# Kernel tuning notes

Hardware: AMD Instinct MI355X
Metric: run time of the kernel (lower is better)

## Reference

```python
import jax, jax.numpy as jnp
import numpy as np

N_NODES = 40000      # batch of group nodes
DEGREE = 32          # neighbors (members) per node
NUM_USERS = 100000
NUM_GROUPS = 50000
EMBED_DIM = 64


def setup_inputs() -> dict:
    key = jax.random.key(0)
    ks = jax.random.split(key, 8)
    E = N_NODES * DEGREE
    d = EMBED_DIM
    return {
        "nodes": jax.random.randint(ks[0], (N_NODES,), 0, NUM_GROUPS),
        "neigh_idx": jax.random.randint(ks[1], (E,), 0, NUM_USERS),
        # edge i belongs to node segment_ids[i]; sorted, DEGREE edges per node
        "segment_ids": jnp.repeat(jnp.arange(N_NODES), DEGREE),
        "u2e_weight": jax.random.normal(ks[2], (NUM_USERS, d), jnp.float32) * 0.02,
        "g2e_weight": jax.random.normal(ks[3], (NUM_GROUPS, d), jnp.float32) * 0.02,
        "att1_w": jax.random.normal(ks[4], (d, 2 * d), jnp.float32) * (1.0 / np.sqrt(2 * d)),
        "att1_b": jnp.zeros((d,), jnp.float32),
        "att2_w": jax.random.normal(ks[5], (d, d), jnp.float32) * (1.0 / np.sqrt(d)),
        "att2_b": jnp.zeros((d,), jnp.float32),
        "att3_w": jax.random.normal(ks[6], (1, d), jnp.float32) * (1.0 / np.sqrt(d)),
        "att3_b": jnp.zeros((1,), jnp.float32),
    }


def _segment_softmax(logits, seg, num_segments):
    # numerically stable softmax within each node's neighbor segment
    m = jax.ops.segment_max(logits, seg, num_segments=num_segments)
    a = jnp.exp(logits - m[seg])
    s = jax.ops.segment_sum(a, seg, num_segments=num_segments)
    return a / s[seg]


def reference(nodes, neigh_idx, segment_ids, u2e_weight, g2e_weight,
              att1_w, att1_b, att2_w, att2_b, att3_w, att3_b):
    e_u = u2e_weight[neigh_idx]                 # [E, d] member embeddings
    g_rep = g2e_weight[nodes][segment_ids]      # [E, d] group query broadcast per edge
    x = jnp.concatenate([e_u, g_rep], axis=-1)  # [E, 2d]
    h = jax.nn.relu(x @ att1_w.T + att1_b)      # [E, d] (dropout inactive at eval)
    h = jax.nn.relu(h @ att2_w.T + att2_b)      # [E, d]
    logits = (h @ att3_w.T + att3_b)[:, 0]      # [E]
    att = _segment_softmax(logits, segment_ids, N_NODES)  # [E]
    # attention-weighted aggregation of member embeddings per node
    return jax.ops.segment_sum(att[:, None] * e_u, segment_ids, num_segments=N_NODES)  # [N, d]
```

## Files before the change

### kernel.cpp

```cpp
#include <hip/hip_runtime.h>
#include <hip/hip_bf16.h>

typedef __attribute__((ext_vector_type(8))) short short8;
typedef __attribute__((ext_vector_type(4))) float floatx4;
typedef __attribute__((ext_vector_type(2))) float float2v;
typedef __attribute__((ext_vector_type(4))) unsigned int uintx4;

#define NNODES 40000
#define NPW 4
#define WAVES 8
#define NPB (NPW * WAVES)
#define NBLK (NNODES / NPB)

#define U2E_ELEMS (100000 * 64)
#define WS_ALIGN 256
#define WS_NEEDED ((size_t)U2E_ELEMS * 2 + WS_ALIGN)


__device__ __forceinline__ float bf2f(unsigned short s) {
    return __uint_as_float(((unsigned int)s) << 16);
}
__device__ __forceinline__ unsigned short f2bf(float f) {
    unsigned int u = __float_as_uint(f);
    u += 0x7fffu + ((u >> 16) & 1u);
    return (unsigned short)(u >> 16);
}
__device__ __forceinline__ unsigned int pk2bf(float lo, float hi) {
#if __has_builtin(__builtin_amdgcn_cvt_pk_bf16_f32)
    auto r = __builtin_amdgcn_cvt_pk_bf16_f32(lo, hi);
    unsigned int u; __builtin_memcpy(&u, &r, 4);
    return u;
#else
    return (unsigned int)f2bf(lo) | ((unsigned int)f2bf(hi) << 16);
#endif
}
__device__ __forceinline__ short8 cvt8(const float* fp) {
    floatx4 a = *(const floatx4*)fp;
    floatx4 b = *(const floatx4*)(fp + 4);
    uintx4 u;
    u[0] = pk2bf(a[0], a[1]); u[1] = pk2bf(a[2], a[3]);
    u[2] = pk2bf(b[0], b[1]); u[3] = pk2bf(b[2], b[3]);
    short8 r; __builtin_memcpy(&r, &u, 16);
    return r;
}
__device__ __forceinline__ short8 u4s8(uintx4 u) {
    short8 r; __builtin_memcpy(&r, &u, 16);
    return r;
}

__device__ __forceinline__ float2v f2pair(floatx4 v, int i) {
    return (float2v){v[2 * i], v[2 * i + 1]};
}
__device__ __forceinline__ float2v fma2(float2v a, float2v b, float2v c) {
#if __has_builtin(__builtin_elementwise_fma)
    return __builtin_elementwise_fma(a, b, c);
#else
    return (float2v){fmaf(a[0], b[0], c[0]), fmaf(a[1], b[1], c[1])};
#endif
}
__device__ __forceinline__ float2v relu2(float2v a) {
#if __has_builtin(__builtin_elementwise_max)
    return __builtin_elementwise_max(a, (float2v)(0.f));
#else
    return (float2v){fmaxf(a[0], 0.f), fmaxf(a[1], 0.f)};
#endif
}

__global__ __launch_bounds__(256) void convert_u2e(
    const float* __restrict__ u2e, unsigned short* __restrict__ ub) {
    const size_t i = ((size_t)blockIdx.x * 256 + threadIdx.x) * 8;
    if (i < U2E_ELEMS) *(short8*)(ub + i) = cvt8(u2e + i);
}

__device__ __forceinline__ int sigma_row(int dt, int m) {
    return (dt & 1) * 32 + (m >> 2) * 8 + ((dt >> 1) << 2) + (m & 3);
}

template<int PRE>
__global__ __launch_bounds__(512, 4) void gat_fused(
    const int*   __restrict__ nodes,
    const int*   __restrict__ neigh,
    const float* __restrict__ u2f,
    const unsigned short* __restrict__ u2b,
    const float* __restrict__ g2e,
    const float* __restrict__ w1,
    const float* __restrict__ b1,
    const float* __restrict__ w2,
    const float* __restrict__ b2,
    const float* __restrict__ w3,
    float* __restrict__ out)
{
    __shared__ alignas(16) short w1f[16 * 64 * 8];
    __shared__ alignas(16) short w2f[8 * 64 * 8];
    __shared__ alignas(16) short ebuf[WAVES][2048];
    __shared__ alignas(16) float abuf[WAVES][64];
    __shared__ alignas(16) float bvec[192];

    const int tid  = threadIdx.x;
    const int wv   = tid >> 6;
    const int lane = tid & 63;
    const int q    = lane >> 4;
    const int n16  = lane & 15;

    for (int i = tid; i < 16 * 64; i += 512) {
        int s = i >> 6, slot = i & 63;
        int dt = s >> 2, kc = s & 3;
        int row = sigma_row(dt, slot & 15);
        int k   = kc * 32 + (slot >> 4) * 8;
        *(short8*)&w1f[i * 8] = cvt8(w1 + (size_t)row * 128 + k);
    }
    for (int i = tid; i < 8 * 64; i += 512) {
        int s = i >> 6, slot = i & 63;
        int ot = s >> 1, kc = s & 1;
        int row = sigma_row(ot, slot & 15);
        int k   = kc * 32 + (slot >> 4) * 8;
        *(short8*)&w2f[i * 8] = cvt8(w2 + (size_t)row * 64 + k);
    }
    for (int i = tid; i < 192; i += 512)
        bvec[i] = (i < 64) ? b1[i] : (i < 128) ? b2[i - 64] : w3[i - 128];
    __syncthreads();

    const int n0 = blockIdx.x * NPB + wv * NPW;

    const int ew0 = n16 * 64 + ((q ^ (n16 & 7)) * 8);
    const int ew1 = n16 * 64 + (((4 + q) ^ (n16 & 7)) * 8);

    const int hh = lane >> 5;
    const int mm = lane & 31;
    int bofs[8];
    #pragma unroll
    for (int p = 0; p < 8; ++p)
        bofs[p] = hh * 1024 + ((((mm >> 2) ^ p) << 3) + ((mm & 3) << 1));
    const int dimo = (mm << 1) | hh;

    int gn, d0, d1;
    short8 A00, A01, A10, A11, G0, G1;

    auto loadA = [&](int idx, int half) -> short8 {
        if (PRE) return *(const short8*)(u2b + (size_t)idx * 64 + half * 32 + q * 8);
        else     return cvt8(u2f + (size_t)idx * 64 + half * 32 + q * 8);
    };

    {
        int g0i = nodes[n0];
        size_t eb0 = (size_t)n0 * 32;
        int c0 = neigh[eb0 + n16];
        int c1 = neigh[eb0 + 16 + n16];
        A00 = loadA(c0, 0); A01 = loadA(c0, 1);
        A10 = loadA(c1, 0); A11 = loadA(c1, 1);
        G0  = cvt8(g2e + (size_t)g0i * 64 + q * 8);
        G1  = cvt8(g2e + (size_t)g0i * 64 + 32 + q * 8);
        int n1 = n0 + 1;
        gn = nodes[n1];
        size_t eb1 = (size_t)n1 * 32;
        d0 = neigh[eb1 + n16];
        d1 = neigh[eb1 + 16 + n16];
    }

    const floatx4 zero4 = {0.f, 0.f, 0.f, 0.f};
    int qo = q * 8;

    for (int it = 0; it < NPW; ++it) {
        const int n = n0 + it;
        const short8 a00 = A00, a01 = A01, a10 = A10, a11 = A11, g0 = G0, g1 = G1;

        floatx4 acc1[2][4];
        #pragma unroll
        for (int et = 0; et < 2; ++et)
            #pragma unroll
            for (int dt = 0; dt < 4; ++dt) acc1[et][dt] = zero4;
        #pragma unroll
        for (int kc = 0; kc < 4; ++kc) {
            const short8 x0 = (kc == 0) ? a00 : (kc == 1) ? a01 : (kc == 2) ? g0 : g1;
            const short8 x1 = (kc == 0) ? a10 : (kc == 1) ? a11 : (kc == 2) ? g0 : g1;
            #pragma unroll
            for (int dt = 0; dt < 4; ++dt) {
                const short8 w = *(const short8*)&w1f[((dt * 4 + kc) * 64 + lane) * 8];
                acc1[0][dt] = __builtin_amdgcn_mfma_f32_16x16x32_bf16(w, x0, acc1[0][dt], 0, 0, 0);
                acc1[1][dt] = __builtin_amdgcn_mfma_f32_16x16x32_bf16(w, x1, acc1[1][dt], 0, 0, 0);
            }
        }

        {
            short* ebw = &ebuf[wv][0];
            *(short8*)&ebw[ew0]        = a00;
            *(short8*)&ebw[ew1]        = a01;
            *(short8*)&ebw[ew0 + 1024] = a10;
            *(short8*)&ebw[ew1 + 1024] = a11;
        }

        if (it < NPW - 1) {
            A00 = loadA(d0, 0); A01 = loadA(d0, 1);
            A10 = loadA(d1, 0); A11 = loadA(d1, 1);
            G0  = cvt8(g2e + (size_t)gn * 64 + qo);
            G1  = cvt8(g2e + (size_t)gn * 64 + 32 + qo);
            int nn = n0 + it + 2; if (nn > NNODES - 1) nn = NNODES - 1;
            gn = nodes[nn];
            size_t eb2 = (size_t)nn * 32;
            d0 = neigh[eb2 + n16];
            d1 = neigh[eb2 + 16 + n16];
        }

        asm volatile("" : "+v"(qo));

        floatx4 B1[2][2];
        B1[0][0] = *(const floatx4*)&bvec[qo];
        B1[0][1] = *(const floatx4*)&bvec[qo + 4];
        B1[1][0] = *(const floatx4*)&bvec[qo + 32];
        B1[1][1] = *(const floatx4*)&bvec[qo + 36];
        short8 y[2][2];
        #pragma unroll
        for (int kc2 = 0; kc2 < 2; ++kc2)
            #pragma unroll
            for (int et = 0; et < 2; ++et) {
                float2v p0 = relu2(f2pair(acc1[et][kc2], 0)     + f2pair(B1[kc2][0], 0));
                float2v p1 = relu2(f2pair(acc1[et][kc2], 1)     + f2pair(B1[kc2][0], 1));
                float2v p2 = relu2(f2pair(acc1[et][kc2 + 2], 0) + f2pair(B1[kc2][1], 0));
                float2v p3 = relu2(f2pair(acc1[et][kc2 + 2], 1) + f2pair(B1[kc2][1], 1));
                uintx4 u;
                u[0] = pk2bf(p0[0], p0[1]);
                u[1] = pk2bf(p1[0], p1[1]);
                u[2] = pk2bf(p2[0], p2[1]);
                u[3] = pk2bf(p3[0], p3[1]);
                y[kc2][et] = u4s8(u);
            }

        floatx4 acc2[2][4];
        #pragma unroll
        for (int et = 0; et < 2; ++et)
            #pragma unroll
            for (int ot = 0; ot < 4; ++ot) acc2[et][ot] = zero4;
        #pragma unroll
        for (int kc2 = 0; kc2 < 2; ++kc2)
            #pragma unroll
            for (int ot = 0; ot < 4; ++ot) {
                const short8 w = *(const short8*)&w2f[((ot * 2 + kc2) * 64 + lane) * 8];
                acc2[0][ot] = __builtin_amdgcn_mfma_f32_16x16x32_bf16(w, y[kc2][0], acc2[0][ot], 0, 0, 0);
                acc2[1][ot] = __builtin_amdgcn_mfma_f32_16x16x32_bf16(w, y[kc2][1], acc2[1][ot], 0, 0, 0);
            }

        floatx4 B2[2][2], W3[2][2];
        B2[0][0] = *(const floatx4*)&bvec[qo + 64];
        B2[0][1] = *(const floatx4*)&bvec[qo + 68];
        B2[1][0] = *(const floatx4*)&bvec[qo + 96];
        B2[1][1] = *(const floatx4*)&bvec[qo + 100];
        W3[0][0] = *(const floatx4*)&bvec[qo + 128];
        W3[0][1] = *(const floatx4*)&bvec[qo + 132];
        W3[1][0] = *(const floatx4*)&bvec[qo + 160];
        W3[1][1] = *(const floatx4*)&bvec[qo + 164];
        float2v s0v = (float2v)(0.f), s1v = (float2v)(0.f);
        #pragma unroll
        for (int ot = 0; ot < 4; ++ot) {
            const int h = ot & 1, g = ot >> 1;
            const float2v b2a = f2pair(B2[h][g], 0), b2b = f2pair(B2[h][g], 1);
            const float2v w3a = f2pair(W3[h][g], 0), w3b = f2pair(W3[h][g], 1);
            s0v = fma2(relu2(f2pair(acc2[0][ot], 0) + b2a), w3a, s0v);
            s0v = fma2(relu2(f2pair(acc2[0][ot], 1) + b2b), w3b, s0v);
            s1v = fma2(relu2(f2pair(acc2[1][ot], 0) + b2a), w3a, s1v);
            s1v = fma2(relu2(f2pair(acc2[1][ot], 1) + b2b), w3b, s1v);
        }
        float s0 = s0v[0] + s0v[1];
        float s1 = s1v[0] + s1v[1];
        s0 += __shfl_xor(s0, 16, 64); s0 += __shfl_xor(s0, 32, 64);
        s1 += __shfl_xor(s1, 16, 64); s1 += __shfl_xor(s1, 32, 64);
        const float lg = ((lane >> 4) & 1) ? s1 : s0;

        float mx = lg;
        #pragma unroll
        for (int off = 1; off < 32; off <<= 1)
            mx = fmaxf(mx, __shfl_xor(mx, off, 64));
        const float ex = __expf(lg - mx);
        float sm = ex;
        #pragma unroll
        for (int off = 1; off < 32; off <<= 1)
            sm += __shfl_xor(sm, off, 64);
        const float attv = ex / sm;

        *(float2v*)&abuf[wv][mm * 2] = (float2v){attv, attv};
        {
            const short* ebw = &ebuf[wv][0];
            const float* abp = &abuf[wv][hh * 32];
            float2v ac0 = (float2v)(0.f), ac1 = (float2v)(0.f);
            #pragma unroll
            for (int k = 0; k < 16; k += 2) {
                const float2v ap0 = *(const float2v*)&abp[2 * k];
                const float2v ap1 = *(const float2v*)&abp[2 * k + 2];
                const unsigned int u0 = *(const unsigned int*)&ebw[bofs[k & 7] + k * 64];
                const unsigned int u1 = *(const unsigned int*)&ebw[bofs[(k + 1) & 7] + (k + 1) * 64];
                float2v e0, e1;
                e0[0] = __uint_as_float(u0 << 16);
                e0[1] = __uint_as_float(u0 & 0xffff0000u);
                e1[0] = __uint_as_float(u1 << 16);
                e1[1] = __uint_as_float(u1 & 0xffff0000u);
                ac0 = fma2(ap0, e0, ac0);
                ac1 = fma2(ap1, e1, ac1);
            }
            const float2v acp = ac0 + ac1;
            const float lt = acp[0] + __shfl_xor(acp[0], 32, 64);
            const float ht = acp[1] + __shfl_xor(acp[1], 32, 64);
            out[(size_t)n * 64 + dimo] = hh ? ht : lt;
        }
    }
}

extern "C" void kernel_launch(void* const* d_in, const int* in_sizes, int n_in,
                              void* d_out, int out_size, void* d_ws, size_t ws_size,
                              hipStream_t stream) {
    const int*   nodes = (const int*)d_in[0];
    const int*   neigh = (const int*)d_in[1];
    const float* u2e = (const float*)d_in[3];
    const float* g2e = (const float*)d_in[4];
    const float* w1  = (const float*)d_in[5];
    const float* b1  = (const float*)d_in[6];
    const float* w2  = (const float*)d_in[7];
    const float* b2  = (const float*)d_in[8];
    const float* w3  = (const float*)d_in[9];
    float* out = (float*)d_out;

    if (ws_size >= WS_NEEDED) {
        unsigned short* ub = (unsigned short*)(((uintptr_t)d_ws + WS_ALIGN - 1) & ~(uintptr_t)(WS_ALIGN - 1));
        hipLaunchKernelGGL(convert_u2e, dim3((U2E_ELEMS / 8 + 255) / 256), dim3(256),
                           0, stream, u2e, ub);
        hipLaunchKernelGGL(gat_fused<1>, dim3(NBLK), dim3(512), 0, stream,
                           nodes, neigh, u2e, ub, g2e, w1, b1, w2, b2, w3, out);
    } else {
        hipLaunchKernelGGL(gat_fused<0>, dim3(NBLK), dim3(512), 0, stream,
                           nodes, neigh, u2e, (const unsigned short*)nullptr,
                           g2e, w1, b1, w2, b2, w3, out);
    }
}
```

Baseline: 155.9 us.

## Precompute bf16 group table and streamline segment softmax reductions

Adds a pre-pass that converts the group embedding table to bf16 in the workspace, so the fused kernel gathers half-width query rows. The softmax drops the max subtraction and uses DPP and swizzle adds plus a hardware reciprocal instead of shuffle-based max and sum reductions. The LDS reads of member embeddings are moved ahead of the softmax so their latency can overlap. The extra conversion pass reads the whole group table each call, and skipping the max subtraction risks overflow for large logits.

```diff
diff --git a/kernel.cpp b/kernel.cpp
--- a/kernel.cpp
+++ b/kernel.cpp
@@ -13,8 +13,10 @@
 #define NBLK (NNODES / NPB)
 
 #define U2E_ELEMS (100000 * 64)
+#define G2E_ELEMS (50000 * 64)
 #define WS_ALIGN 256
-#define WS_NEEDED ((size_t)U2E_ELEMS * 2 + WS_ALIGN)
+#define WS_NEEDED   ((size_t)U2E_ELEMS * 2 + WS_ALIGN)
+#define WS_NEEDED_G ((size_t)U2E_ELEMS * 2 + (size_t)G2E_ELEMS * 2 + WS_ALIGN)
 
 
 __device__ __forceinline__ float bf2f(unsigned short s) {
@@ -66,23 +68,47 @@
 #endif
 }
 
+template<int CTRL>
+__device__ __forceinline__ float dppadd(float v) {
+#if __has_builtin(__builtin_amdgcn_update_dpp)
+    int y = __builtin_amdgcn_update_dpp(0, __float_as_int(v), CTRL, 0xf, 0xf, true);
+    return v + __int_as_float(y);
+#else
+    return v + __shfl_xor(v, (CTRL == 0xB1) ? 1 : (CTRL == 0x4E) ? 2 : (CTRL == 0x141) ? 4 : 8, 64);
+#endif
+}
+__device__ __forceinline__ float swz16add(float v) {
+#if __has_builtin(__builtin_amdgcn_ds_swizzle)
+    int y = __builtin_amdgcn_ds_swizzle(__float_as_int(v), 0x401F);
+    return v + __int_as_float(y);
+#else
+    return v + __shfl_xor(v, 16, 64);
+#endif
+}
+
 __global__ __launch_bounds__(256) void convert_u2e(
     const float* __restrict__ u2e, unsigned short* __restrict__ ub) {
     const size_t i = ((size_t)blockIdx.x * 256 + threadIdx.x) * 8;
     if (i < U2E_ELEMS) *(short8*)(ub + i) = cvt8(u2e + i);
 }
+__global__ __launch_bounds__(256) void convert_g2e(
+    const float* __restrict__ g2e, unsigned short* __restrict__ gb) {
+    const size_t i = ((size_t)blockIdx.x * 256 + threadIdx.x) * 8;
+    if (i < G2E_ELEMS) *(short8*)(gb + i) = cvt8(g2e + i);
+}
 
 __device__ __forceinline__ int sigma_row(int dt, int m) {
     return (dt & 1) * 32 + (m >> 2) * 8 + ((dt >> 1) << 2) + (m & 3);
 }
 
-template<int PRE>
+template<int PRE, int GPRE>
 __global__ __launch_bounds__(512, 4) void gat_fused(
     const int*   __restrict__ nodes,
     const int*   __restrict__ neigh,
     const float* __restrict__ u2f,
     const unsigned short* __restrict__ u2b,
     const float* __restrict__ g2e,
+    const unsigned short* __restrict__ g2b,
     const float* __restrict__ w1,
     const float* __restrict__ b1,
     const float* __restrict__ w2,
@@ -140,6 +166,10 @@
         if (PRE) return *(const short8*)(u2b + (size_t)idx * 64 + half * 32 + q * 8);
         else     return cvt8(u2f + (size_t)idx * 64 + half * 32 + q * 8);
     };
+    auto loadG = [&](int gi, int half, int qoff) -> short8 {
+        if (GPRE) return *(const short8*)(g2b + (size_t)gi * 64 + half * 32 + qoff);
+        else      return cvt8(g2e + (size_t)gi * 64 + half * 32 + qoff);
+    };
 
     {
         int g0i = nodes[n0];
@@ -148,8 +178,8 @@
         int c1 = neigh[eb0 + 16 + n16];
         A00 = loadA(c0, 0); A01 = loadA(c0, 1);
         A10 = loadA(c1, 0); A11 = loadA(c1, 1);
-        G0  = cvt8(g2e + (size_t)g0i * 64 + q * 8);
-        G1  = cvt8(g2e + (size_t)g0i * 64 + 32 + q * 8);
+        G0  = loadG(g0i, 0, q * 8);
+        G1  = loadG(g0i, 1, q * 8);
         int n1 = n0 + 1;
         gn = nodes[n1];
         size_t eb1 = (size_t)n1 * 32;
@@ -192,8 +222,8 @@
         if (it < NPW - 1) {
             A00 = loadA(d0, 0); A01 = loadA(d0, 1);
             A10 = loadA(d1, 0); A11 = loadA(d1, 1);
-            G0  = cvt8(g2e + (size_t)gn * 64 + qo);
-            G1  = cvt8(g2e + (size_t)gn * 64 + 32 + qo);
+            G0  = loadG(gn, 0, qo);
+            G1  = loadG(gn, 1, qo);
             int nn = n0 + it + 2; if (nn > NNODES - 1) nn = NNODES - 1;
             gn = nodes[nn];
             size_t eb2 = (size_t)nn * 32;
@@ -265,28 +295,34 @@
         s1 += __shfl_xor(s1, 16, 64); s1 += __shfl_xor(s1, 32, 64);
         const float lg = ((lane >> 4) & 1) ? s1 : s0;
 
-        float mx = lg;
-        #pragma unroll
-        for (int off = 1; off < 32; off <<= 1)
-            mx = fmaxf(mx, __shfl_xor(mx, off, 64));
-        const float ex = __expf(lg - mx);
-        float sm = ex;
-        #pragma unroll
-        for (int off = 1; off < 32; off <<= 1)
-            sm += __shfl_xor(sm, off, 64);
+        const short* ebw = &ebuf[wv][0];
+        unsigned int eu[16];
+        #pragma unroll
+        for (int k = 0; k < 16; ++k)
+            eu[k] = *(const unsigned int*)&ebw[bofs[k & 7] + k * 64];
+
+        const float ex = __expf(lg);
+        float sm = dppadd<0xB1>(ex);
+        sm = dppadd<0x4E>(sm);
+        sm = dppadd<0x141>(sm);
+        sm = dppadd<0x140>(sm);
+        sm = swz16add(sm);
+#if __has_builtin(__builtin_amdgcn_rcpf)
+        const float attv = ex * __builtin_amdgcn_rcpf(sm);
+#else
         const float attv = ex / sm;
+#endif
 
         *(float2v*)&abuf[wv][mm * 2] = (float2v){attv, attv};
         {
-            const short* ebw = &ebuf[wv][0];
             const float* abp = &abuf[wv][hh * 32];
             float2v ac0 = (float2v)(0.f), ac1 = (float2v)(0.f);
             #pragma unroll
             for (int k = 0; k < 16; k += 2) {
                 const float2v ap0 = *(const float2v*)&abp[2 * k];
                 const float2v ap1 = *(const float2v*)&abp[2 * k + 2];
-                const unsigned int u0 = *(const unsigned int*)&ebw[bofs[k & 7] + k * 64];
-                const unsigned int u1 = *(const unsigned int*)&ebw[bofs[(k + 1) & 7] + (k + 1) * 64];
+                const unsigned int u0 = eu[k];
+                const unsigned int u1 = eu[k + 1];
                 float2v e0, e1;
                 e0[0] = __uint_as_float(u0 << 16);
                 e0[1] = __uint_as_float(u0 & 0xffff0000u);
@@ -317,15 +353,26 @@
     const float* w3  = (const float*)d_in[9];
     float* out = (float*)d_out;
 
-    if (ws_size >= WS_NEEDED) {
-        unsigned short* ub = (unsigned short*)(((uintptr_t)d_ws + WS_ALIGN - 1) & ~(uintptr_t)(WS_ALIGN - 1));
+    unsigned short* ub = (unsigned short*)(((uintptr_t)d_ws + WS_ALIGN - 1) & ~(uintptr_t)(WS_ALIGN - 1));
+    unsigned short* gb = ub + U2E_ELEMS;
+
+    if (ws_size >= WS_NEEDED_G) {
         hipLaunchKernelGGL(convert_u2e, dim3((U2E_ELEMS / 8 + 255) / 256), dim3(256),
                            0, stream, u2e, ub);
-        hipLaunchKernelGGL(gat_fused<1>, dim3(NBLK), dim3(512), 0, stream,
-                           nodes, neigh, u2e, ub, g2e, w1, b1, w2, b2, w3, out);
+        hipLaunchKernelGGL(convert_g2e, dim3((G2E_ELEMS / 8 + 255) / 256), dim3(256),
+                           0, stream, g2e, gb);
+        hipLaunchKernelGGL((gat_fused<1, 1>), dim3(NBLK), dim3(512), 0, stream,
+                           nodes, neigh, u2e, ub, g2e, gb, w1, b1, w2, b2, w3, out);
+    } else if (ws_size >= WS_NEEDED) {
+        hipLaunchKernelGGL(convert_u2e, dim3((U2E_ELEMS / 8 + 255) / 256), dim3(256),
+                           0, stream, u2e, ub);
+        hipLaunchKernelGGL((gat_fused<1, 0>), dim3(NBLK), dim3(512), 0, stream,
+                           nodes, neigh, u2e, ub, g2e, (const unsigned short*)nullptr,
+                           w1, b1, w2, b2, w3, out);
     } else {
-        hipLaunchKernelGGL(gat_fused<0>, dim3(NBLK), dim3(512), 0, stream,
+        hipLaunchKernelGGL((gat_fused<0, 0>), dim3(NBLK), dim3(512), 0, stream,
                            nodes, neigh, u2e, (const unsigned short*)nullptr,
-                           g2e, w1, b1, w2, b2, w3, out);
-    }
-}
+                           g2e, (const unsigned short*)nullptr,
+                           w1, b1, w2, b2, w3, out);
+    }
+}
```

New measurement: 159.7 us. 1.02x slower.

## Software-pipeline next node's layer-1 MFMAs behind softmax, use DPP reductions

Applied to the files above, without the earlier changes.

Restructures the per-wave node loop so the layer-1 MFMA for the next node is issued while the current node's softmax and aggregation run. The current node's member embeddings are read from LDS into registers before the next node's embeddings overwrite that buffer, and the loop is fully unrolled. The softmax drops the max subtraction and does its sum with DPP and ds_swizzle instead of shuffles, plus a fast reciprocal in place of the divide. This hides MFMA latency and cuts cross-lane reduction cost, at the price of more registers and no overflow protection for large logits.

```diff
diff --git a/kernel.cpp b/kernel.cpp
--- a/kernel.cpp
+++ b/kernel.cpp
@@ -63,6 +63,24 @@
     return __builtin_elementwise_max(a, (float2v)(0.f));
 #else
     return (float2v){fmaxf(a[0], 0.f), fmaxf(a[1], 0.f)};
+#endif
+}
+
+template<int CTRL>
+__device__ __forceinline__ float dppadd(float v) {
+#if __has_builtin(__builtin_amdgcn_update_dpp)
+    int y = __builtin_amdgcn_update_dpp(0, __float_as_int(v), CTRL, 0xf, 0xf, true);
+    return v + __int_as_float(y);
+#else
+    return v + __shfl_xor(v, (CTRL == 0xB1) ? 1 : (CTRL == 0x4E) ? 2 : (CTRL == 0x141) ? 4 : 8, 64);
+#endif
+}
+__device__ __forceinline__ float swz16add(float v) {
+#if __has_builtin(__builtin_amdgcn_ds_swizzle)
+    int y = __builtin_amdgcn_ds_swizzle(__float_as_int(v), 0x401F);
+    return v + __int_as_float(y);
+#else
+    return v + __shfl_xor(v, 16, 64);
 #endif
 }
 
@@ -141,6 +159,9 @@
         else     return cvt8(u2f + (size_t)idx * 64 + half * 32 + q * 8);
     };
 
+    const floatx4 zero4 = {0.f, 0.f, 0.f, 0.f};
+    floatx4 acc1cur[2][4];
+
     {
         int g0i = nodes[n0];
         size_t eb0 = (size_t)n0 * 32;
@@ -155,52 +176,45 @@
         size_t eb1 = (size_t)n1 * 32;
         d0 = neigh[eb1 + n16];
         d1 = neigh[eb1 + 16 + n16];
-    }
-
-    const floatx4 zero4 = {0.f, 0.f, 0.f, 0.f};
+
+        #pragma unroll
+        for (int et = 0; et < 2; ++et)
+            #pragma unroll
+            for (int dt = 0; dt < 4; ++dt) acc1cur[et][dt] = zero4;
+        #pragma unroll
+        for (int kc = 0; kc < 4; ++kc) {
+            const short8 x0 = (kc == 0) ? A00 : (kc == 1) ? A01 : (kc == 2) ? G0 : G1;
+            const short8 x1 = (kc == 0) ? A10 : (kc == 1) ? A11 : (kc == 2) ? G0 : G1;
+            #pragma unroll
+            for (int dt = 0; dt < 4; ++dt) {
+                const short8 w = *(const short8*)&w1f[((dt * 4 + kc) * 64 + lane) * 8];
+                acc1cur[0][dt] = __builtin_amdgcn_mfma_f32_16x16x32_bf16(w, x0, acc1cur[0][dt], 0, 0, 0);
+                acc1cur[1][dt] = __builtin_amdgcn_mfma_f32_16x16x32_bf16(w, x1, acc1cur[1][dt], 0, 0, 0);
+            }
+        }
+        {
+            short* ebw = &ebuf[wv][0];
+            *(short8*)&ebw[ew0]        = A00;
+            *(short8*)&ebw[ew1]        = A01;
+            *(short8*)&ebw[ew0 + 1024] = A10;
+            *(short8*)&ebw[ew1 + 1024] = A11;
+        }
+        A00 = loadA(d0, 0); A01 = loadA(d0, 1);
+        A10 = loadA(d1, 0); A11 = loadA(d1, 1);
+        G0  = cvt8(g2e + (size_t)gn * 64 + q * 8);
+        G1  = cvt8(g2e + (size_t)gn * 64 + 32 + q * 8);
+        int n2 = n0 + 2; if (n2 > NNODES - 1) n2 = NNODES - 1;
+        gn = nodes[n2];
+        size_t eb2 = (size_t)n2 * 32;
+        d0 = neigh[eb2 + n16];
+        d1 = neigh[eb2 + 16 + n16];
+    }
+
     int qo = q * 8;
 
+    #pragma unroll
     for (int it = 0; it < NPW; ++it) {
         const int n = n0 + it;
-        const short8 a00 = A00, a01 = A01, a10 = A10, a11 = A11, g0 = G0, g1 = G1;
-
-        floatx4 acc1[2][4];
-        #pragma unroll
-        for (int et = 0; et < 2; ++et)
-            #pragma unroll
-            for (int dt = 0; dt < 4; ++dt) acc1[et][dt] = zero4;
-        #pragma unroll
-        for (int kc = 0; kc < 4; ++kc) {
-            const short8 x0 = (kc == 0) ? a00 : (kc == 1) ? a01 : (kc == 2) ? g0 : g1;
-            const short8 x1 = (kc == 0) ? a10 : (kc == 1) ? a11 : (kc == 2) ? g0 : g1;
-            #pragma unroll
-            for (int dt = 0; dt < 4; ++dt) {
-                const short8 w = *(const short8*)&w1f[((dt * 4 + kc) * 64 + lane) * 8];
-                acc1[0][dt] = __builtin_amdgcn_mfma_f32_16x16x32_bf16(w, x0, acc1[0][dt], 0, 0, 0);
-                acc1[1][dt] = __builtin_amdgcn_mfma_f32_16x16x32_bf16(w, x1, acc1[1][dt], 0, 0, 0);
-            }
-        }
-
-        {
-            short* ebw = &ebuf[wv][0];
-            *(short8*)&ebw[ew0]        = a00;
-            *(short8*)&ebw[ew1]        = a01;
-            *(short8*)&ebw[ew0 + 1024] = a10;
-            *(short8*)&ebw[ew1 + 1024] = a11;
-        }
-
-        if (it < NPW - 1) {
-            A00 = loadA(d0, 0); A01 = loadA(d0, 1);
-            A10 = loadA(d1, 0); A11 = loadA(d1, 1);
-            G0  = cvt8(g2e + (size_t)gn * 64 + qo);
-            G1  = cvt8(g2e + (size_t)gn * 64 + 32 + qo);
-            int nn = n0 + it + 2; if (nn > NNODES - 1) nn = NNODES - 1;
-            gn = nodes[nn];
-            size_t eb2 = (size_t)nn * 32;
-            d0 = neigh[eb2 + n16];
-            d1 = neigh[eb2 + 16 + n16];
-        }
-
         asm volatile("" : "+v"(qo));
 
         floatx4 B1[2][2];
@@ -213,10 +227,10 @@
         for (int kc2 = 0; kc2 < 2; ++kc2)
             #pragma unroll
             for (int et = 0; et < 2; ++et) {
-                float2v p0 = relu2(f2pair(acc1[et][kc2], 0)     + f2pair(B1[kc2][0], 0));
-                float2v p1 = relu2(f2pair(acc1[et][kc2], 1)     + f2pair(B1[kc2][0], 1));
-                float2v p2 = relu2(f2pair(acc1[et][kc2 + 2], 0) + f2pair(B1[kc2][1], 0));
-                float2v p3 = relu2(f2pair(acc1[et][kc2 + 2], 1) + f2pair(B1[kc2][1], 1));
+                float2v p0 = relu2(f2pair(acc1cur[et][kc2], 0)     + f2pair(B1[kc2][0], 0));
+                float2v p1 = relu2(f2pair(acc1cur[et][kc2], 1)     + f2pair(B1[kc2][0], 1));
+                float2v p2 = relu2(f2pair(acc1cur[et][kc2 + 2], 0) + f2pair(B1[kc2][1], 0));
+                float2v p3 = relu2(f2pair(acc1cur[et][kc2 + 2], 1) + f2pair(B1[kc2][1], 1));
                 uintx4 u;
                 u[0] = pk2bf(p0[0], p0[1]);
                 u[1] = pk2bf(p1[0], p1[1]);
@@ -265,28 +279,69 @@
         s1 += __shfl_xor(s1, 16, 64); s1 += __shfl_xor(s1, 32, 64);
         const float lg = ((lane >> 4) & 1) ? s1 : s0;
 
-        float mx = lg;
-        #pragma unroll
-        for (int off = 1; off < 32; off <<= 1)
-            mx = fmaxf(mx, __shfl_xor(mx, off, 64));
-        const float ex = __expf(lg - mx);
-        float sm = ex;
-        #pragma unroll
-        for (int off = 1; off < 32; off <<= 1)
-            sm += __shfl_xor(sm, off, 64);
+        const short* ebw = &ebuf[wv][0];
+        unsigned int eu[16];
+        #pragma unroll
+        for (int k = 0; k < 16; ++k)
+            eu[k] = *(const unsigned int*)&ebw[bofs[k & 7] + k * 64];
+
+        floatx4 acc1nxt[2][4];
+        if (it < NPW - 1) {
+            #pragma unroll
+            for (int et = 0; et < 2; ++et)
+                #pragma unroll
+                for (int dt = 0; dt < 4; ++dt) acc1nxt[et][dt] = zero4;
+            #pragma unroll
+            for (int kc = 0; kc < 4; ++kc) {
+                const short8 x0 = (kc == 0) ? A00 : (kc == 1) ? A01 : (kc == 2) ? G0 : G1;
+                const short8 x1 = (kc == 0) ? A10 : (kc == 1) ? A11 : (kc == 2) ? G0 : G1;
+                #pragma unroll
+                for (int dt = 0; dt < 4; ++dt) {
+                    const short8 w = *(const short8*)&w1f[((dt * 4 + kc) * 64 + lane) * 8];
+                    acc1nxt[0][dt] = __builtin_amdgcn_mfma_f32_16x16x32_bf16(w, x0, acc1nxt[0][dt], 0, 0, 0);
+                    acc1nxt[1][dt] = __builtin_amdgcn_mfma_f32_16x16x32_bf16(w, x1, acc1nxt[1][dt], 0, 0, 0);
+                }
+            }
+            {
+                short* ebw2 = &ebuf[wv][0];
+                *(short8*)&ebw2[ew0]        = A00;
+                *(short8*)&ebw2[ew1]        = A01;
+                *(short8*)&ebw2[ew0 + 1024] = A10;
+                *(short8*)&ebw2[ew1 + 1024] = A11;
+            }
+            A00 = loadA(d0, 0); A01 = loadA(d0, 1);
+            A10 = loadA(d1, 0); A11 = loadA(d1, 1);
+            G0  = cvt8(g2e + (size_t)gn * 64 + qo);
+            G1  = cvt8(g2e + (size_t)gn * 64 + 32 + qo);
+            int nn = n0 + it + 3; if (nn > NNODES - 1) nn = NNODES - 1;
+            gn = nodes[nn];
+            size_t eb2 = (size_t)nn * 32;
+            d0 = neigh[eb2 + n16];
+            d1 = neigh[eb2 + 16 + n16];
+        }
+
+        const float ex = __expf(lg);
+        float sm = dppadd<0xB1>(ex);
+        sm = dppadd<0x4E>(sm);
+        sm = dppadd<0x141>(sm);
+        sm = dppadd<0x140>(sm);
+        sm = swz16add(sm);
+#if __has_builtin(__builtin_amdgcn_rcpf)
+        const float attv = ex * __builtin_amdgcn_rcpf(sm);
+#else
         const float attv = ex / sm;
+#endif
 
         *(float2v*)&abuf[wv][mm * 2] = (float2v){attv, attv};
         {
-            const short* ebw = &ebuf[wv][0];
             const float* abp = &abuf[wv][hh * 32];
             float2v ac0 = (float2v)(0.f), ac1 = (float2v)(0.f);
             #pragma unroll
             for (int k = 0; k < 16; k += 2) {
                 const float2v ap0 = *(const float2v*)&abp[2 * k];
                 const float2v ap1 = *(const float2v*)&abp[2 * k + 2];
-                const unsigned int u0 = *(const unsigned int*)&ebw[bofs[k & 7] + k * 64];
-                const unsigned int u1 = *(const unsigned int*)&ebw[bofs[(k + 1) & 7] + (k + 1) * 64];
+                const unsigned int u0 = eu[k];
+                const unsigned int u1 = eu[k + 1];
                 float2v e0, e1;
                 e0[0] = __uint_as_float(u0 << 16);
                 e0[1] = __uint_as_float(u0 & 0xffff0000u);
@@ -299,6 +354,13 @@
             const float lt = acp[0] + __shfl_xor(acp[0], 32, 64);
             const float ht = acp[1] + __shfl_xor(acp[1], 32, 64);
             out[(size_t)n * 64 + dimo] = hh ? ht : lt;
+        }
+
+        if (it < NPW - 1) {
+            #pragma unroll
+            for (int et = 0; et < 2; ++et)
+                #pragma unroll
+                for (int dt = 0; dt < 4; ++dt) acc1cur[et][dt] = acc1nxt[et][dt];
         }
     }
 }
```

After: 163.2 us. 4.7% more time.
